# Kernel optimization log

Hardware: AMD Instinct MI355X
Metric: run time of the kernel (lower is better)

The kernel has to match this reference:

```python
import jax, jax.numpy as jnp
import numpy as np

N, E, F, D, L, G, T = 100000, 600000, 64, 128, 3, 256, 10
BN_EPS = 1e-5


def _bn(x, g, b):
    # training-mode BatchNorm1d over all rows (biased variance)
    m = x.mean(0)
    v = jnp.mean((x - m) ** 2, 0)
    return (x - m) * jax.lax.rsqrt(v + BN_EPS) * g + b


def _masked_bn(x, mask, g, b):
    # BatchNorm1d computed only over rows where mask==1 (target nodes),
    # matching torch's nn(s[target_nodes_id]) which normalizes the subset.
    cnt = jnp.maximum(mask.sum(), 1.0)
    m = (mask[:, None] * x).sum(0) / cnt
    v = (mask[:, None] * (x - m) ** 2).sum(0) / cnt
    return (x - m) * jax.lax.rsqrt(v + BN_EPS) * g + b


def setup_inputs() -> dict:
    key = jax.random.key(0)
    ks = jax.random.split(key, 32)
    inp = {}
    inp["dag_x"] = jax.random.normal(ks[0], (N, F), dtype=jnp.float32)
    inp["dag_edge_index"] = jax.random.randint(ks[1], (2, E), 0, N)
    inp["edge_multiplicities"] = jax.random.uniform(ks[2], (E,), dtype=jnp.float32)
    inp["dag_layers_mask"] = jax.random.randint(ks[3], (E,), 0, L)
    inp["batch"] = jnp.sort(jax.random.randint(ks[4], (N,), 0, G))
    inp["leaves0"] = jax.random.randint(ks[5], (50000,), 0, N)
    inp["readouts"] = jax.random.randint(ks[6], (L + 1, 20000), 0, N)
    # node_features_transformation params
    inp["W1"] = jax.random.normal(ks[7], (F, D), dtype=jnp.float32) / np.sqrt(F)
    inp["b1"] = jnp.zeros((D,), jnp.float32)
    inp["g1"] = jnp.ones((D,), jnp.float32)
    inp["be1"] = jnp.zeros((D,), jnp.float32)
    inp["W2"] = jax.random.normal(ks[8], (D, D), dtype=jnp.float32) / np.sqrt(D)
    inp["b2"] = jnp.zeros((D,), jnp.float32)
    inp["g2"] = jnp.ones((D,), jnp.float32)
    inp["be2"] = jnp.zeros((D,), jnp.float32)
    # per-DAG-layer MLP params (stacked over L layers)
    inp["dag_W1"] = jax.random.normal(ks[9], (L, D, D), dtype=jnp.float32) / np.sqrt(D)
    inp["dag_b1"] = jnp.zeros((L, D), jnp.float32)
    inp["dag_g1"] = jnp.ones((L, D), jnp.float32)
    inp["dag_be1"] = jnp.zeros((L, D), jnp.float32)
    inp["dag_W2"] = jax.random.normal(ks[10], (L, D, D), dtype=jnp.float32) / np.sqrt(D)
    inp["dag_b2"] = jnp.zeros((L, D), jnp.float32)
    inp["dag_g2"] = jnp.ones((L, D), jnp.float32)
    inp["dag_be2"] = jnp.zeros((L, D), jnp.float32)
    inp["dag_eps"] = jnp.zeros((L,), jnp.float32)
    # readout linear (last_layer)
    inp["Wl"] = jax.random.normal(ks[11], (D, T), dtype=jnp.float32) / np.sqrt(D)
    inp["bl"] = jnp.zeros((T,), jnp.float32)
    return inp


def reference(dag_x, edge_multiplicities, W1, b1, g1, be1, W2, b2, g2, be2,
              dag_W1, dag_b1, dag_g1, dag_be1, dag_W2, dag_b2, dag_g2, dag_be2,
              dag_eps, Wl, bl, dag_edge_index, dag_layers_mask, batch, leaves0,
              readouts):
    # node feature transformation: Linear-BN-ReLU x2
    feature = jax.nn.relu(_bn(dag_x @ W1 + b1, g1, be1))
    feature = jax.nn.relu(_bn(feature @ W2 + b2, g2, be2))
    # x starts as zeros except on layer-0 leaves
    x = jnp.zeros_like(feature).at[leaves0].set(feature[leaves0])
    src, dst = dag_edge_index[0], dag_edge_index[1]
    for i in range(L):
        active = (dag_layers_mask == i)
        w = jnp.where(active, edge_multiplicities, 0.0)  # [E]
        # weighted gather-scatter message passing (inactive edges contribute 0)
        E_X = jax.ops.segment_sum(x[src] * w[:, None], dst, num_segments=N)
        tcnt = jax.ops.segment_sum(active.astype(jnp.float32), dst, num_segments=N)
        is_t = (tcnt > 0).astype(x.dtype)  # [N] target-node mask
        # self-loop term (1+eps)*feature only on targets, plus aggregated messages
        s = is_t[:, None] * ((1.0 + dag_eps[i]) * feature) + E_X
        h = jax.nn.relu(_masked_bn(s @ dag_W1[i] + dag_b1[i], is_t, dag_g1[i], dag_be1[i]))
        h = jax.nn.relu(_masked_bn(h @ dag_W2[i] + dag_b2[i], is_t, dag_g2[i], dag_be2[i]))
        # MLP applied only on target nodes, then residual add of x
        x = jnp.where(is_t[:, None] > 0, h, s) + x
    # multi-height readout: sum-pool per graph at each height, then mean over heights
    pooled = []
    for i in range(L + 1):
        idx = readouts[i]
        pooled.append(jax.ops.segment_sum(x[idx], batch[idx], num_segments=G))
    out = jnp.stack(pooled, 1).mean(1) @ Wl + bl  # [G, T]
    return out
```

## Files before the change

kernel.cpp:

```cpp
#include <hip/hip_runtime.h>

constexpr int Nn = 100000;
constexpr int Ee = 600000;
constexpr int Dd = 128;
constexpr int Ll = 3;
constexpr int Gg = 256;
constexpr int Tt = 10;
constexpr float BN_EPS = 1e-5f;
constexpr int NREP = 16;
constexpr int PSL = 8;
constexpr int PR = 32;

typedef __attribute__((ext_vector_type(8))) short short8v;
typedef __attribute__((ext_vector_type(4))) float f32x4;

__device__ inline ushort bf_hi(float f) {
  unsigned u = __float_as_uint(f);
  unsigned r = (u + 0x7FFFu + ((u >> 16) & 1u)) >> 16;
  return (ushort)r;
}
__device__ inline float bf_f(ushort h) {
  return __uint_as_float(((unsigned)h) << 16);
}

__device__ inline void compute_ss_lds(const float* __restrict__ stats,
                                      const float* __restrict__ g,
                                      const float* __restrict__ be, float cnt,
                                      float* ssS) {
  const int c = threadIdx.x;
  if (c < 128) {
    float S = 0.f, Q = 0.f;
#pragma unroll
    for (int r = 0; r < NREP; ++r) {
      S += stats[r * 512 + c];
      Q += stats[r * 512 + 256 + c];
    }
    const float m = S / cnt;
    const float v = Q / cnt - m * m;
    const float sc = g[c] * rsqrtf(v + BN_EPS);
    ssS[c] = sc;
    ssS[128 + c] = be[c] - m * sc;
  }
}

template <bool NORM_A, bool MASKED>
__global__ __launch_bounds__(256, 4) void gemm_bf16(
    const ushort* __restrict__ A, const ushort* __restrict__ WTh,
    const ushort* __restrict__ WTl, const float* __restrict__ bias,
    const float* __restrict__ statsIn, const float* __restrict__ gN,
    const float* __restrict__ beN, const float* __restrict__ cntPtr,
    const int* __restrict__ tmask, ushort* __restrict__ C,
    float* __restrict__ statsOut, int nrows) {
  __shared__ ushort SB[16384];
  __shared__ float ssS[256];
  ushort* Bh = SB;
  ushort* Bl = SB + 8192;
  const int tid = threadIdx.x;
  const int w = tid >> 6, lane = tid & 63, lr = lane & 15, lg = lane >> 4;
  const int rt = blockIdx.x >> 1, ct = blockIdx.x & 1;
  const int rowBase = rt * 128, cBase = ct * 64;
  const int rep = blockIdx.x & (NREP - 1);

  {
    const int cc = tid >> 2;
    const ushort* sH = WTh + (size_t)(cBase + cc) * 128;
    const ushort* sL = WTl + (size_t)(cBase + cc) * 128;
    char* BhB = (char*)Bh;
    char* BlB = (char*)Bl;
#pragma unroll
    for (int i = 0; i < 4; ++i) {
      const int slot = (tid & 3) * 4 + i;
      const int off = (cc * 256 + slot * 16) ^ ((cc & 7) << 4);
      *(short8v*)(BhB + off) = *(const short8v*)(sH + slot * 8);
      *(short8v*)(BlB + off) = *(const short8v*)(sL + slot * 8);
    }
  }
  if (NORM_A) {
    const float cnt = cntPtr ? fmaxf(cntPtr[0], 1.f) : (float)nrows;
    compute_ss_lds(statsIn, gN, beN, cnt, ssS);
  }

  const int row0 = rowBase + w * 32 + lr;
  const int row1 = row0 + 16;
  const bool ok0 = row0 < nrows, ok1 = row1 < nrows;
  const short8v szero = {0, 0, 0, 0, 0, 0, 0, 0};
  const ushort* aP0 = A + (size_t)row0 * 128 + lg * 8;
  const ushort* aP1 = A + (size_t)row1 * 128 + lg * 8;
  short8v ar0[4], ar1[4];
#pragma unroll
  for (int c = 0; c < 4; ++c) {
    ar0[c] = ok0 ? *(const short8v*)(aP0 + c * 32) : szero;
    ar1[c] = ok1 ? *(const short8v*)(aP1 + c * 32) : szero;
  }
  __syncthreads();

  const f32x4 fzero = {0.f, 0.f, 0.f, 0.f};
  f32x4 acc[2][4];
#pragma unroll
  for (int i = 0; i < 2; ++i)
#pragma unroll
    for (int j = 0; j < 4; ++j) acc[i][j] = fzero;

  const char* BhB = (const char*)Bh;
  const char* BlB = (const char*)Bl;
  __builtin_amdgcn_s_setprio(1);
#pragma unroll
  for (int c = 0; c < 4; ++c) {
    short8v a0 = ar0[c], a1 = ar1[c];
    if (NORM_A) {
      const int kb = c * 32 + lg * 8;
      const float4 s0 = *(const float4*)&ssS[kb];
      const float4 s1 = *(const float4*)&ssS[kb + 4];
      const float4 h0 = *(const float4*)&ssS[128 + kb];
      const float4 h1 = *(const float4*)&ssS[128 + kb + 4];
      const float sv[8] = {s0.x, s0.y, s0.z, s0.w, s1.x, s1.y, s1.z, s1.w};
      const float hv[8] = {h0.x, h0.y, h0.z, h0.w, h1.x, h1.y, h1.z, h1.w};
#pragma unroll
      for (int j = 0; j < 8; ++j) {
        a0[j] = (short)bf_hi(fmaxf(fmaf(bf_f((ushort)a0[j]), sv[j], hv[j]), 0.f));
        a1[j] = (short)bf_hi(fmaxf(fmaf(bf_f((ushort)a1[j]), sv[j], hv[j]), 0.f));
      }
    }
#pragma unroll
    for (int nf = 0; nf < 4; ++nf) {
      const int brow = nf * 16 + lr;
      const int off = (brow * 256 + (c * 4 + lg) * 16) ^ ((lr & 7) << 4);
      const short8v bh = *(const short8v*)(BhB + off);
      const short8v bl = *(const short8v*)(BlB + off);
      acc[0][nf] = __builtin_amdgcn_mfma_f32_16x16x32_bf16(a0, bh, acc[0][nf], 0, 0, 0);
      acc[1][nf] = __builtin_amdgcn_mfma_f32_16x16x32_bf16(a1, bh, acc[1][nf], 0, 0, 0);
      acc[0][nf] = __builtin_amdgcn_mfma_f32_16x16x32_bf16(a0, bl, acc[0][nf], 0, 0, 0);
      acc[1][nf] = __builtin_amdgcn_mfma_f32_16x16x32_bf16(a1, bl, acc[1][nf], 0, 0, 0);
    }
  }
  __builtin_amdgcn_s_setprio(0);

  float mrow[2][4];
#pragma unroll
  for (int mf = 0; mf < 2; ++mf)
#pragma unroll
    for (int rr = 0; rr < 4; ++rr) {
      const int row = rowBase + w * 32 + mf * 16 + lg * 4 + rr;
      float m = 0.f;
      if (row < nrows) m = MASKED ? ((tmask[row] > 0) ? 1.f : 0.f) : 1.f;
      mrow[mf][rr] = m;
    }
  __syncthreads();
  ushort* Cs = SB;
  float* Sred = (float*)(SB + 9216);
  float* Sq = Sred + 256;
#pragma unroll
  for (int nf = 0; nf < 4; ++nf) {
    const int col = nf * 16 + lr;
    const float bcol = bias[cBase + col];
    float ps = 0.f, pq = 0.f;
#pragma unroll
    for (int mf = 0; mf < 2; ++mf) {
      const f32x4 vv = acc[mf][nf];
#pragma unroll
      for (int rr = 0; rr < 4; ++rr) {
        const float o = vv[rr] + bcol;
        const int rl = w * 32 + mf * 16 + lg * 4 + rr;
        Cs[rl * 72 + col] = bf_hi(o);
        const float mo = mrow[mf][rr] * o;
        ps += mo;
        pq += mo * o;
      }
    }
    ps += __shfl_xor(ps, 16);
    ps += __shfl_xor(ps, 32);
    pq += __shfl_xor(pq, 16);
    pq += __shfl_xor(pq, 32);
    if (lg == 0) {
      Sred[w * 64 + col] = ps;
      Sq[w * 64 + col] = pq;
    }
  }
  __syncthreads();
  {
    const int rl = tid >> 1, half = tid & 1;
    const int grow = rowBase + rl;
    if (grow < nrows) {
      ushort* dstp = C + (size_t)grow * 128 + cBase + half * 32;
      const ushort* srcp = Cs + rl * 72 + half * 32;
#pragma unroll
      for (int j = 0; j < 4; ++j)
        *(short8v*)(dstp + j * 8) = *(const short8v*)(srcp + j * 8);
    }
  }
  if (tid < 64) {
    float s = 0.f;
#pragma unroll
    for (int q = 0; q < 4; ++q) s += Sred[q * 64 + tid];
    atomicAdd(&statsOut[rep * 512 + cBase + tid], s);
  } else if (tid < 128) {
    float s = 0.f;
#pragma unroll
    for (int q = 0; q < 4; ++q) s += Sq[q * 64 + tid - 64];
    atomicAdd(&statsOut[rep * 512 + 256 + cBase + tid - 64], s);
  }
}

__global__ __launch_bounds__(256, 4) void gemm_f32a(
    const float* __restrict__ A, const ushort* __restrict__ WTh,
    const ushort* __restrict__ WTl, const float* __restrict__ bias,
    ushort* __restrict__ C, float* __restrict__ statsOut, int nrows) {
  __shared__ ushort SB[11264];
  ushort* Bh = SB;
  ushort* Bl = SB + 4096;
  const int tid = threadIdx.x;
  const int w = tid >> 6, lane = tid & 63, lr = lane & 15, lg = lane >> 4;
  const int rt = blockIdx.x >> 1, ct = blockIdx.x & 1;
  const int rowBase = rt * 128, cBase = ct * 64;
  const int rep = blockIdx.x & (NREP - 1);

  {
    const int cc = tid >> 2;
    const ushort* sH = WTh + (size_t)(cBase + cc) * 64;
    const ushort* sL = WTl + (size_t)(cBase + cc) * 64;
    char* BhB = (char*)Bh;
    char* BlB = (char*)Bl;
#pragma unroll
    for (int i = 0; i < 2; ++i) {
      const int slot = (tid & 3) * 2 + i;
      const int off = (cc * 128 + slot * 16) ^ ((cc & 7) << 4);
      *(short8v*)(BhB + off) = *(const short8v*)(sH + slot * 8);
      *(short8v*)(BlB + off) = *(const short8v*)(sL + slot * 8);
    }
  }

  const int row0 = rowBase + w * 32 + lr;
  const int row1 = row0 + 16;
  const bool ok0 = row0 < nrows, ok1 = row1 < nrows;
  const float4 fz4 = make_float4(0.f, 0.f, 0.f, 0.f);
  const float* aP0 = A + (size_t)row0 * 64 + lg * 8;
  const float* aP1 = A + (size_t)row1 * 64 + lg * 8;
  float4 ar0[2][2], ar1[2][2];
#pragma unroll
  for (int c = 0; c < 2; ++c) {
    ar0[c][0] = ok0 ? *(const float4*)(aP0 + c * 32) : fz4;
    ar0[c][1] = ok0 ? *(const float4*)(aP0 + c * 32 + 4) : fz4;
    ar1[c][0] = ok1 ? *(const float4*)(aP1 + c * 32) : fz4;
    ar1[c][1] = ok1 ? *(const float4*)(aP1 + c * 32 + 4) : fz4;
  }
  __syncthreads();

  const f32x4 fzero = {0.f, 0.f, 0.f, 0.f};
  f32x4 acc[2][4];
#pragma unroll
  for (int i = 0; i < 2; ++i)
#pragma unroll
    for (int j = 0; j < 4; ++j) acc[i][j] = fzero;

  const char* BhB = (const char*)Bh;
  const char* BlB = (const char*)Bl;
  __builtin_amdgcn_s_setprio(1);
#pragma unroll
  for (int c = 0; c < 2; ++c) {
    const float v0[8] = {ar0[c][0].x, ar0[c][0].y, ar0[c][0].z, ar0[c][0].w,
                         ar0[c][1].x, ar0[c][1].y, ar0[c][1].z, ar0[c][1].w};
    const float v1[8] = {ar1[c][0].x, ar1[c][0].y, ar1[c][0].z, ar1[c][0].w,
                         ar1[c][1].x, ar1[c][1].y, ar1[c][1].z, ar1[c][1].w};
    short8v a0h, a0l, a1h, a1l;
#pragma unroll
    for (int j = 0; j < 8; ++j) {
      ushort hh = bf_hi(v0[j]);
      a0h[j] = (short)hh;
      a0l[j] = (short)bf_hi(v0[j] - bf_f(hh));
      hh = bf_hi(v1[j]);
      a1h[j] = (short)hh;
      a1l[j] = (short)bf_hi(v1[j] - bf_f(hh));
    }
#pragma unroll
    for (int nf = 0; nf < 4; ++nf) {
      const int brow = nf * 16 + lr;
      const int off = (brow * 128 + (c * 4 + lg) * 16) ^ ((lr & 7) << 4);
      const short8v bh = *(const short8v*)(BhB + off);
      const short8v bl = *(const short8v*)(BlB + off);
      acc[0][nf] = __builtin_amdgcn_mfma_f32_16x16x32_bf16(a0h, bh, acc[0][nf], 0, 0, 0);
      acc[1][nf] = __builtin_amdgcn_mfma_f32_16x16x32_bf16(a1h, bh, acc[1][nf], 0, 0, 0);
      acc[0][nf] = __builtin_amdgcn_mfma_f32_16x16x32_bf16(a0l, bh, acc[0][nf], 0, 0, 0);
      acc[1][nf] = __builtin_amdgcn_mfma_f32_16x16x32_bf16(a1l, bh, acc[1][nf], 0, 0, 0);
      acc[0][nf] = __builtin_amdgcn_mfma_f32_16x16x32_bf16(a0h, bl, acc[0][nf], 0, 0, 0);
      acc[1][nf] = __builtin_amdgcn_mfma_f32_16x16x32_bf16(a1h, bl, acc[1][nf], 0, 0, 0);
    }
  }
  __builtin_amdgcn_s_setprio(0);

  __syncthreads();
  ushort* Cs = SB;
  float* Sred = (float*)(SB + 9216);
  float* Sq = Sred + 256;
#pragma unroll
  for (int nf = 0; nf < 4; ++nf) {
    const int col = nf * 16 + lr;
    const float bcol = bias[cBase + col];
    float ps = 0.f, pq = 0.f;
#pragma unroll
    for (int mf = 0; mf < 2; ++mf) {
      const f32x4 vv = acc[mf][nf];
#pragma unroll
      for (int rr = 0; rr < 4; ++rr) {
        const float o = vv[rr] + bcol;
        const int rl = w * 32 + mf * 16 + lg * 4 + rr;
        Cs[rl * 72 + col] = bf_hi(o);
        const int row = rowBase + rl;
        const float m = (row < nrows) ? 1.f : 0.f;
        const float mo = m * o;
        ps += mo;
        pq += mo * o;
      }
    }
    ps += __shfl_xor(ps, 16);
    ps += __shfl_xor(ps, 32);
    pq += __shfl_xor(pq, 16);
    pq += __shfl_xor(pq, 32);
    if (lg == 0) {
      Sred[w * 64 + col] = ps;
      Sq[w * 64 + col] = pq;
    }
  }
  __syncthreads();
  {
    const int rl = tid >> 1, half = tid & 1;
    const int grow = rowBase + rl;
    if (grow < nrows) {
      ushort* dstp = C + (size_t)grow * 128 + cBase + half * 32;
      const ushort* srcp = Cs + rl * 72 + half * 32;
#pragma unroll
      for (int j = 0; j < 4; ++j)
        *(short8v*)(dstp + j * 8) = *(const short8v*)(srcp + j * 8);
    }
  }
  if (tid < 64) {
    float s = 0.f;
#pragma unroll
    for (int q = 0; q < 4; ++q) s += Sred[q * 64 + tid];
    atomicAdd(&statsOut[rep * 512 + cBase + tid], s);
  } else if (tid < 128) {
    float s = 0.f;
#pragma unroll
    for (int q = 0; q < 4; ++q) s += Sq[q * 64 + tid - 64];
    atomicAdd(&statsOut[rep * 512 + 256 + cBase + tid - 64], s);
  }
}

__global__ __launch_bounds__(256) void wsplit_kernel(
    const float* __restrict__ W1, const float* __restrict__ W2,
    const float* __restrict__ dW1, const float* __restrict__ dW2,
    ushort* __restrict__ wsT) {
  const int t = blockIdx.x * 256 + threadIdx.x;
  const int slot = t >> 14;
  const int idx = t & 16383;
  if (slot >= 8) return;
  const int Ks = (slot == 0) ? 64 : 128;
  if (idx >= 128 * Ks) return;
  const int c = idx / Ks;
  const int k = idx - c * Ks;
  float v;
  if (slot == 0) v = W1[k * 128 + c];
  else if (slot == 1) v = W2[k * 128 + c];
  else if (slot < 5) v = dW1[(slot - 2) * 16384 + k * 128 + c];
  else v = dW2[(slot - 5) * 16384 + k * 128 + c];
  const ushort h = bf_hi(v);
  const ushort l = bf_hi(v - bf_f(h));
  wsT[slot * 32768 + c * Ks + k] = h;
  wsT[slot * 32768 + 16384 + c * Ks + k] = l;
}

__global__ __launch_bounds__(256) void normrelu_kernel(
    const ushort* __restrict__ in, const float* __restrict__ stats,
    const float* __restrict__ g, const float* __restrict__ be, float cntFixed,
    ushort* __restrict__ outp) {
  __shared__ float ssS[256];
  compute_ss_lds(stats, g, be, cntFixed, ssS);
  __syncthreads();
  const int tid = threadIdx.x;
  const int c4 = (tid & 31) * 4;
  const float4 sc = *(const float4*)&ssS[c4];
  const float4 sh = *(const float4*)&ssS[128 + c4];
  const int rowBase = blockIdx.x * 64;
#pragma unroll
  for (int it = 0; it < 8; ++it) {
    const int row = rowBase + it * 8 + (tid >> 5);
    if (row >= Nn) continue;
    const size_t idx = (size_t)row * 32 + (tid & 31);
    const ushort4 v = ((const ushort4*)in)[idx];
    ushort4 o;
    o.x = bf_hi(fmaxf(fmaf(bf_f(v.x), sc.x, sh.x), 0.f));
    o.y = bf_hi(fmaxf(fmaf(bf_f(v.y), sc.y, sh.y), 0.f));
    o.z = bf_hi(fmaxf(fmaf(bf_f(v.z), sc.z, sh.z), 0.f));
    o.w = bf_hi(fmaxf(fmaf(bf_f(v.w), sc.w, sh.w), 0.f));
    ((ushort4*)outp)[idx] = o;
  }
}

__global__ __launch_bounds__(256) void normrelu_acc_kernel(
    const ushort* __restrict__ in, const float* __restrict__ stats,
    const float* __restrict__ g, const float* __restrict__ be,
    const float* __restrict__ cntPtr, const int* __restrict__ tmask,
    ushort* __restrict__ x) {
  __shared__ float ssS[256];
  compute_ss_lds(stats, g, be, fmaxf(cntPtr[0], 1.f), ssS);
  __syncthreads();
  const int tid = threadIdx.x;
  const int c4 = (tid & 31) * 4;
  const float4 sc = *(const float4*)&ssS[c4];
  const float4 sh = *(const float4*)&ssS[128 + c4];
  const int rowBase = blockIdx.x * 64;
#pragma unroll
  for (int it = 0; it < 8; ++it) {
    const int row = rowBase + it * 8 + (tid >> 5);
    if (row >= Nn || tmask[row] <= 0) continue;
    const size_t idx = (size_t)row * 32 + (tid & 31);
    const ushort4 v = ((const ushort4*)in)[idx];
    ushort4 xo = ((const ushort4*)x)[idx];
    xo.x = bf_hi(bf_f(xo.x) + fmaxf(fmaf(bf_f(v.x), sc.x, sh.x), 0.f));
    xo.y = bf_hi(bf_f(xo.y) + fmaxf(fmaf(bf_f(v.y), sc.y, sh.y), 0.f));
    xo.z = bf_hi(bf_f(xo.z) + fmaxf(fmaf(bf_f(v.z), sc.z, sh.z), 0.f));
    xo.w = bf_hi(bf_f(xo.w) + fmaxf(fmaf(bf_f(v.w), sc.w, sh.w), 0.f));
    ((ushort4*)x)[idx] = xo;
  }
}

__global__ __launch_bounds__(256) void scatter_leaves_kernel(
    const int* __restrict__ leaves, const ushort* __restrict__ feat,
    ushort* __restrict__ x, int nl) {
  const int gid = blockIdx.x * 256 + threadIdx.x;
  const int j = gid >> 5;
  if (j >= nl) return;
  const int node = leaves[j];
  const int c4 = (gid & 31) * 4;
  *(ushort4*)&x[(size_t)node * 128 + c4] =
      *(const ushort4*)&feat[(size_t)node * 128 + c4];
}

__global__ __launch_bounds__(256) void deg_count_kernel(
    const int* __restrict__ dst, const int* __restrict__ lmask,
    int* __restrict__ cnts) {
  const int e = blockIdx.x * 256 + threadIdx.x;
  if (e >= Ee) return;
  atomicAdd(&cnts[lmask[e] * Nn + dst[e]], 1);
}

__global__ __launch_bounds__(256) void scan1_kernel(const int* __restrict__ in,
                                                    int* __restrict__ out,
                                                    int* __restrict__ bsum,
                                                    float* __restrict__ tcountf,
                                                    int n) {
  __shared__ int lds[256];
  __shared__ float tcS[3];
  const int tid = threadIdx.x;
  const int base = blockIdx.x * 2048 + tid * 8;
  int vals[8];
  int tsum = 0;
  float t0 = 0.f, t1 = 0.f, t2 = 0.f;
#pragma unroll
  for (int j = 0; j < 8; ++j) {
    const int i = base + j;
    const int v = (i < n) ? in[i] : 0;
    if (v > 0) {
      if (i < Nn) t0 += 1.f;
      else if (i < 2 * Nn) t1 += 1.f;
      else t2 += 1.f;
    }
    vals[j] = tsum;
    tsum += v;
  }
  lds[tid] = tsum;
  if (tid < 3) tcS[tid] = 0.f;
  __syncthreads();
  if (t0 != 0.f) atomicAdd(&tcS[0], t0);
  if (t1 != 0.f) atomicAdd(&tcS[1], t1);
  if (t2 != 0.f) atomicAdd(&tcS[2], t2);
  for (int off = 1; off < 256; off <<= 1) {
    const int y = (tid >= off) ? lds[tid - off] : 0;
    __syncthreads();
    lds[tid] += y;
    __syncthreads();
  }
  const int texcl = (tid > 0) ? lds[tid - 1] : 0;
#pragma unroll
  for (int j = 0; j < 8; ++j)
    if (base + j < n) out[base + j] = texcl + vals[j];
  if (tid == 255) bsum[blockIdx.x] = lds[255];
  __syncthreads();
  if (tid < 3 && tcS[tid] != 0.f) atomicAdd(&tcountf[tid], tcS[tid]);
}

__global__ void scan2_kernel(int* __restrict__ bsum, int nb) {
  __shared__ int lds[256];
  const int tid = threadIdx.x;
  const int v = (tid < nb) ? bsum[tid] : 0;
  lds[tid] = v;
  __syncthreads();
  for (int off = 1; off < 256; off <<= 1) {
    const int y = (tid >= off) ? lds[tid - off] : 0;
    __syncthreads();
    lds[tid] += y;
    __syncthreads();
  }
  if (tid < nb) bsum[tid] = lds[tid] - v;
}

__global__ __launch_bounds__(256) void scan3_kernel(int* __restrict__ out,
                                                    int* __restrict__ cursor,
                                                    const int* __restrict__ bsum,
                                                    int n, int etot) {
  const int i = blockIdx.x * 256 + threadIdx.x;
  if (i >= n) return;
  const int v = out[i] + bsum[i >> 11];
  out[i] = v;
  cursor[i] = v;
  if (i == n - 1) out[n] = etot;
}

__global__ __launch_bounds__(256) void csr_fill_kernel(
    const int* __restrict__ src, const int* __restrict__ dst,
    const float* __restrict__ mult, const int* __restrict__ lmask,
    int* __restrict__ cursor, int2* __restrict__ pairs) {
  const int e = blockIdx.x * 256 + threadIdx.x;
  if (e >= Ee) return;
  const int slot = atomicAdd(&cursor[lmask[e] * Nn + dst[e]], 1);
  pairs[slot] = make_int2(src[e], __float_as_int(mult[e]));
}

__global__ __launch_bounds__(256) void agg_kernel(
    const int* __restrict__ offs, const int2* __restrict__ pairs,
    const ushort* __restrict__ x, const ushort* __restrict__ feat,
    const float* __restrict__ deps, int layer, ushort* __restrict__ sbuf,
    int* __restrict__ tmask) {
  const int node = blockIdx.x * 4 + (threadIdx.x >> 6);
  const int lane = threadIdx.x & 63;
  const int gi = layer * Nn + node;
  const int o0 = offs[gi];
  const int o1 = offs[gi + 1];
  ushort2 fv = make_ushort2(0, 0);
  if (o1 > o0) fv = *(const ushort2*)&feat[(size_t)node * 128 + lane * 2];
  float ax = 0.f, ay = 0.f;
  for (int p = o0; p < o1; p += 2) {
    const int2 pr0 = pairs[p];
    const int2 pr1 = (p + 1 < o1) ? pairs[p + 1] : make_int2(0, 0);
    const ushort2 x0 = *(const ushort2*)&x[(size_t)pr0.x * 128 + lane * 2];
    const ushort2 x1 = *(const ushort2*)&x[(size_t)pr1.x * 128 + lane * 2];
    const float w0 = __int_as_float(pr0.y);
    const float w1 = __int_as_float(pr1.y);
    ax = fmaf(w0, bf_f(x0.x), ax);
    ay = fmaf(w0, bf_f(x0.y), ay);
    ax = fmaf(w1, bf_f(x1.x), ax);
    ay = fmaf(w1, bf_f(x1.y), ay);
  }
  if (o1 > o0) {
    const float c = 1.f + deps[layer];
    ax = fmaf(c, bf_f(fv.x), ax);
    ay = fmaf(c, bf_f(fv.y), ay);
  }
  ushort2 o;
  o.x = bf_hi(ax);
  o.y = bf_hi(ay);
  *(ushort2*)&sbuf[(size_t)node * 128 + lane * 2] = o;
  if (lane == 0) tmask[node] = (o1 > o0) ? 1 : 0;
}

__global__ __launch_bounds__(256) void phist_kernel(const int* __restrict__ ridx,
                                                    const int* __restrict__ batch,
                                                    int* __restrict__ cnt, int n) {
  const int i = blockIdx.x * 256 + threadIdx.x;
  if (i >= n) return;
  atomicAdd(&cnt[batch[ridx[i]] * PR + (i & (PR - 1))], 1);
}

__global__ void pscan_kernel(int* __restrict__ cnt, int* __restrict__ cur) {
  __shared__ int l[256];
  const int t = threadIdx.x;
  const int base = t * 32;
  int vals[32];
  int tsum = 0;
#pragma unroll
  for (int j = 0; j < 32; ++j) {
    const int v = cnt[base + j];
    vals[j] = tsum;
    tsum += v;
  }
  l[t] = tsum;
  __syncthreads();
  for (int off = 1; off < 256; off <<= 1) {
    const int y = (t >= off) ? l[t - off] : 0;
    __syncthreads();
    l[t] += y;
    __syncthreads();
  }
  const int excl = (t > 0) ? l[t - 1] : 0;
#pragma unroll
  for (int j = 0; j < 32; ++j) {
    const int v = excl + vals[j];
    cnt[base + j] = v;
    cur[base + j] = v;
  }
}

__global__ __launch_bounds__(256) void pfill_kernel(const int* __restrict__ ridx,
                                                    const int* __restrict__ batch,
                                                    int* __restrict__ cur,
                                                    int* __restrict__ sorted,
                                                    int n) {
  const int i = blockIdx.x * 256 + threadIdx.x;
  if (i >= n) return;
  const int node = ridx[i];
  const int slot = atomicAdd(&cur[batch[node] * PR + (i & (PR - 1))], 1);
  sorted[slot] = node;
}

__global__ __launch_bounds__(256) void ppool_kernel(const int* __restrict__ sorted,
                                                    const int* __restrict__ offs,
                                                    const ushort* __restrict__ x,
                                                    float* __restrict__ Ppart,
                                                    int n) {
  __shared__ float part[4][256];
  const int bid = blockIdx.x;
  const int g = bid >> 3, slice = bid & (PSL - 1);
  const int w = threadIdx.x >> 6;
  const int lane = threadIdx.x & 63;
  const int o0 = offs[g * PR];
  const int o1 = (g < Gg - 1) ? offs[(g + 1) * PR] : n;
  float ax = 0.f, ay = 0.f;
  for (int p = o0 + slice * 4 + w; p < o1; p += 32) {
    const int node = sorted[p];
    const ushort2 xv = *(const ushort2*)&x[(size_t)node * 128 + lane * 2];
    ax += bf_f(xv.x);
    ay += bf_f(xv.y);
  }
  part[w][lane * 2] = ax;
  part[w][lane * 2 + 1] = ay;
  __syncthreads();
  if (threadIdx.x < 128) {
    const int c = threadIdx.x;
    Ppart[(size_t)bid * 128 + c] =
        part[0][c] + part[1][c] + part[2][c] + part[3][c];
  }
}

__global__ __launch_bounds__(256) void preduce_kernel(
    const float* __restrict__ Ppart, float* __restrict__ P) {
  const int gid = blockIdx.x * 256 + threadIdx.x;
  const int g = gid >> 7, c = gid & 127;
  float s = 0.f;
#pragma unroll
  for (int t = 0; t < PSL; ++t) s += Ppart[(size_t)(g * PSL + t) * 128 + c];
  P[gid] = s;
}

__global__ void out_kernel(const float* __restrict__ P,
                           const float* __restrict__ Wl,
                           const float* __restrict__ bl,
                           float* __restrict__ out) {
  const int gid = blockIdx.x * blockDim.x + threadIdx.x;
  if (gid >= Gg * Tt) return;
  const int g = gid / Tt;
  const int t = gid - g * Tt;
  float acc = 0.f;
  for (int c = 0; c < 128; ++c) acc += P[g * 128 + c] * Wl[c * Tt + t];
  out[gid] = acc * 0.25f + bl[t];
}

extern "C" void kernel_launch(void* const* d_in, const int* in_sizes, int n_in,
                              void* d_out, int out_size, void* d_ws,
                              size_t ws_size, hipStream_t stream) {
  const float* dag_x = (const float*)d_in[0];
  const int* eidx = (const int*)d_in[1];
  const int* src = eidx;
  const int* dst = eidx + Ee;
  const float* mult = (const float*)d_in[2];
  const int* lmask = (const int*)d_in[3];
  const int* batch = (const int*)d_in[4];
  const int* leaves = (const int*)d_in[5];
  const int* readouts = (const int*)d_in[6];
  const float* W1 = (const float*)d_in[7];
  const float* b1 = (const float*)d_in[8];
  const float* g1 = (const float*)d_in[9];
  const float* be1 = (const float*)d_in[10];
  const float* W2 = (const float*)d_in[11];
  const float* b2 = (const float*)d_in[12];
  const float* g2 = (const float*)d_in[13];
  const float* be2 = (const float*)d_in[14];
  const float* dW1 = (const float*)d_in[15];
  const float* db1 = (const float*)d_in[16];
  const float* dg1 = (const float*)d_in[17];
  const float* dbe1 = (const float*)d_in[18];
  const float* dW2 = (const float*)d_in[19];
  const float* db2 = (const float*)d_in[20];
  const float* dg2 = (const float*)d_in[21];
  const float* dbe2 = (const float*)d_in[22];
  const float* deps = (const float*)d_in[23];
  const float* Wl = (const float*)d_in[24];
  const float* bl = (const float*)d_in[25];
  float* out = (float*)d_out;

  const size_t ND = (size_t)Nn * Dd;
  ushort* feat = (ushort*)d_ws;
  ushort* xbuf = feat + ND;
  ushort* Abuf = xbuf + ND;
  ushort* Bbuf = Abuf + ND;
  float* statsAll = (float*)(Bbuf + ND);
  float* tcountf = statsAll + 8 * 8192;
  int* tmask = (int*)(tcountf + 8);
  ushort* wsT = (ushort*)(tmask + Nn);
  int* offs = (int*)(wsT + 262144);
  int2* pairs = (int2*)(offs + 3 * Nn + 4);

  int* cnts = (int*)xbuf;
  int* cursor = cnts + 3 * Nn;
  int* bsum = cursor + 3 * Nn;
  const int nridx = in_sizes[6];
  const int nleaves = in_sizes[5];
  int* pcnt = (int*)Abuf;
  int* pcur = pcnt + Gg * PR;
  int* sorted = pcur + Gg * PR;
  float* Ppart = (float*)(sorted + nridx);
  float* P = Ppart + Gg * PSL * 128;

  dim3 blk(256);
  hipMemsetAsync(statsAll, 0, (8 * 8192 + 8) * sizeof(float), stream);
  wsplit_kernel<<<512, blk, 0, stream>>>(W1, W2, dW1, dW2, wsT);

  hipMemsetAsync(cnts, 0, 3 * Nn * sizeof(int), stream);
  deg_count_kernel<<<2344, blk, 0, stream>>>(dst, lmask, cnts);
  scan1_kernel<<<147, blk, 0, stream>>>(cnts, offs, bsum, tcountf, 3 * Nn);
  scan2_kernel<<<1, blk, 0, stream>>>(bsum, 147);
  scan3_kernel<<<1172, blk, 0, stream>>>(offs, cursor, bsum, 3 * Nn, Ee);
  csr_fill_kernel<<<2344, blk, 0, stream>>>(src, dst, mult, lmask, cursor, pairs);

  const int gGemm = 782 * 2;
  gemm_f32a<<<gGemm, blk, 0, stream>>>(dag_x, wsT, wsT + 16384, b1, Abuf,
                                       statsAll + 0 * 8192, Nn);
  gemm_bf16<true, false><<<gGemm, blk, 0, stream>>>(
      Abuf, wsT + 32768, wsT + 32768 + 16384, b2, statsAll + 0 * 8192, g1, be1,
      nullptr, nullptr, Bbuf, statsAll + 1 * 8192, Nn);
  normrelu_kernel<<<1563, blk, 0, stream>>>(Bbuf, statsAll + 1 * 8192, g2, be2,
                                            (float)Nn, feat);

  hipMemsetAsync(xbuf, 0, ND * sizeof(ushort), stream);
  scatter_leaves_kernel<<<6250, blk, 0, stream>>>(leaves, feat, xbuf, nleaves);

  for (int layer = 0; layer < Ll; ++layer) {
    agg_kernel<<<25000, blk, 0, stream>>>(offs, pairs, xbuf, feat, deps, layer,
                                          Abuf, tmask);
    const int so1 = (2 + layer) * 32768;
    const int so2 = (5 + layer) * 32768;
    const int po = layer * Dd;
    float* st1 = statsAll + (size_t)(2 + 2 * layer) * 8192;
    float* st2 = statsAll + (size_t)(3 + 2 * layer) * 8192;
    gemm_bf16<false, true><<<gGemm, blk, 0, stream>>>(
        Abuf, wsT + so1, wsT + so1 + 16384, db1 + po, nullptr, nullptr,
        nullptr, nullptr, tmask, Bbuf, st1, Nn);
    gemm_bf16<true, true><<<gGemm, blk, 0, stream>>>(
        Bbuf, wsT + so2, wsT + so2 + 16384, db2 + po, st1, dg1 + po, dbe1 + po,
        tcountf + layer, tmask, Abuf, st2, Nn);
    normrelu_acc_kernel<<<1563, blk, 0, stream>>>(
        Abuf, st2, dg2 + po, dbe2 + po, tcountf + layer, tmask, xbuf);
  }

  hipMemsetAsync(pcnt, 0, Gg * PR * sizeof(int), stream);
  const int gIdx = (nridx + 255) / 256;
  phist_kernel<<<gIdx, blk, 0, stream>>>(readouts, batch, pcnt, nridx);
  pscan_kernel<<<1, blk, 0, stream>>>(pcnt, pcur);
  pfill_kernel<<<gIdx, blk, 0, stream>>>(readouts, batch, pcur, sorted, nridx);
  ppool_kernel<<<Gg * PSL, blk, 0, stream>>>(sorted, pcnt, xbuf, Ppart, nridx);
  preduce_kernel<<<Gg * 128 / 256, blk, 0, stream>>>(Ppart, P);
  out_kernel<<<10, blk, 0, stream>>>(P, Wl, bl, out);
}
```

Measured before the change: 498.2 us.

## Fuse neighbor aggregation into first DAG GEMM and merge small scan/output kernels

Adds a gemm_agg kernel that gathers weighted neighbor rows and the self-loop term directly into MFMA A-fragments in registers, replacing the separate agg_kernel and its write and re-read of the aggregated buffer. It also folds the xbuf zeroing into normrelu_kernel, merges scan2 into scan3 (each block redoes the small block-sum scan), and fuses preduce and out_kernel into one pout_kernel. These changes remove intermediate global traffic and several launches. In exchange, each GEMM block does irregular gathers with one lane-group per row, which may load-imbalance and stall the MFMA pipeline on high-degree nodes.

```diff
diff --git a/kernel.cpp b/kernel.cpp
--- a/kernel.cpp
+++ b/kernel.cpp
@@ -144,6 +144,222 @@
       float m = 0.f;
       if (row < nrows) m = MASKED ? ((tmask[row] > 0) ? 1.f : 0.f) : 1.f;
       mrow[mf][rr] = m;
+    }
+  __syncthreads();
+  ushort* Cs = SB;
+  float* Sred = (float*)(SB + 9216);
+  float* Sq = Sred + 256;
+#pragma unroll
+  for (int nf = 0; nf < 4; ++nf) {
+    const int col = nf * 16 + lr;
+    const float bcol = bias[cBase + col];
+    float ps = 0.f, pq = 0.f;
+#pragma unroll
+    for (int mf = 0; mf < 2; ++mf) {
+      const f32x4 vv = acc[mf][nf];
+#pragma unroll
+      for (int rr = 0; rr < 4; ++rr) {
+        const float o = vv[rr] + bcol;
+        const int rl = w * 32 + mf * 16 + lg * 4 + rr;
+        Cs[rl * 72 + col] = bf_hi(o);
+        const float mo = mrow[mf][rr] * o;
+        ps += mo;
+        pq += mo * o;
+      }
+    }
+    ps += __shfl_xor(ps, 16);
+    ps += __shfl_xor(ps, 32);
+    pq += __shfl_xor(pq, 16);
+    pq += __shfl_xor(pq, 32);
+    if (lg == 0) {
+      Sred[w * 64 + col] = ps;
+      Sq[w * 64 + col] = pq;
+    }
+  }
+  __syncthreads();
+  {
+    const int rl = tid >> 1, half = tid & 1;
+    const int grow = rowBase + rl;
+    if (grow < nrows) {
+      ushort* dstp = C + (size_t)grow * 128 + cBase + half * 32;
+      const ushort* srcp = Cs + rl * 72 + half * 32;
+#pragma unroll
+      for (int j = 0; j < 4; ++j)
+        *(short8v*)(dstp + j * 8) = *(const short8v*)(srcp + j * 8);
+    }
+  }
+  if (tid < 64) {
+    float s = 0.f;
+#pragma unroll
+    for (int q = 0; q < 4; ++q) s += Sred[q * 64 + tid];
+    atomicAdd(&statsOut[rep * 512 + cBase + tid], s);
+  } else if (tid < 128) {
+    float s = 0.f;
+#pragma unroll
+    for (int q = 0; q < 4; ++q) s += Sq[q * 64 + tid - 64];
+    atomicAdd(&statsOut[rep * 512 + 256 + cBase + tid - 64], s);
+  }
+}
+
+__global__ __launch_bounds__(256, 4) void gemm_agg(
+    const ushort* __restrict__ x, const ushort* __restrict__ feat,
+    const int* __restrict__ offs, const int2* __restrict__ pairs,
+    const float* __restrict__ deps, int layer, const ushort* __restrict__ WTh,
+    const ushort* __restrict__ WTl, const float* __restrict__ bias,
+    ushort* __restrict__ C, float* __restrict__ statsOut,
+    int* __restrict__ tmask, int nrows) {
+  __shared__ ushort SB[16384];
+  ushort* Bh = SB;
+  ushort* Bl = SB + 8192;
+  const int tid = threadIdx.x;
+  const int w = tid >> 6, lane = tid & 63, lr = lane & 15, lg = lane >> 4;
+  const int rt = blockIdx.x >> 1, ct = blockIdx.x & 1;
+  const int rowBase = rt * 128, cBase = ct * 64;
+  const int rep = blockIdx.x & (NREP - 1);
+
+  {
+    const int cc = tid >> 2;
+    const ushort* sH = WTh + (size_t)(cBase + cc) * 128;
+    const ushort* sL = WTl + (size_t)(cBase + cc) * 128;
+    char* BhB = (char*)Bh;
+    char* BlB = (char*)Bl;
+#pragma unroll
+    for (int i = 0; i < 4; ++i) {
+      const int slot = (tid & 3) * 4 + i;
+      const int off = (cc * 256 + slot * 16) ^ ((cc & 7) << 4);
+      *(short8v*)(BhB + off) = *(const short8v*)(sH + slot * 8);
+      *(short8v*)(BlB + off) = *(const short8v*)(sL + slot * 8);
+    }
+  }
+
+  const float ce = 1.f + deps[layer];
+  const int row0 = rowBase + w * 32 + lr;
+  const int row1 = row0 + 16;
+  int o0a = 0, o1a = 0, o0b = 0, o1b = 0;
+  if (row0 < nrows) {
+    o0a = offs[layer * Nn + row0];
+    o1a = offs[layer * Nn + row0 + 1];
+  }
+  if (row1 < nrows) {
+    o0b = offs[layer * Nn + row1];
+    o1b = offs[layer * Nn + row1 + 1];
+  }
+  if (lg == 0) {
+    if (row0 < nrows) tmask[row0] = (o1a > o0a) ? 1 : 0;
+    if (row1 < nrows) tmask[row1] = (o1b > o0b) ? 1 : 0;
+  }
+
+  short8v ar0[4], ar1[4];
+  {
+    float a[4][8];
+#pragma unroll
+    for (int c = 0; c < 4; ++c)
+#pragma unroll
+      for (int j = 0; j < 8; ++j) a[c][j] = 0.f;
+    for (int p = o0a; p < o1a; ++p) {
+      const int2 pr = pairs[p];
+      const float wgt = __int_as_float(pr.y);
+      const ushort* xr = x + (size_t)pr.x * 128 + lg * 8;
+#pragma unroll
+      for (int c = 0; c < 4; ++c) {
+        const short8v xv = *(const short8v*)(xr + c * 32);
+#pragma unroll
+        for (int j = 0; j < 8; ++j)
+          a[c][j] = fmaf(wgt, bf_f((ushort)xv[j]), a[c][j]);
+      }
+    }
+    if (o1a > o0a) {
+      const ushort* fr = feat + (size_t)row0 * 128 + lg * 8;
+#pragma unroll
+      for (int c = 0; c < 4; ++c) {
+        const short8v fv = *(const short8v*)(fr + c * 32);
+#pragma unroll
+        for (int j = 0; j < 8; ++j)
+          a[c][j] = fmaf(ce, bf_f((ushort)fv[j]), a[c][j]);
+      }
+    }
+#pragma unroll
+    for (int c = 0; c < 4; ++c)
+#pragma unroll
+      for (int j = 0; j < 8; ++j) ar0[c][j] = (short)bf_hi(a[c][j]);
+  }
+  {
+    float a[4][8];
+#pragma unroll
+    for (int c = 0; c < 4; ++c)
+#pragma unroll
+      for (int j = 0; j < 8; ++j) a[c][j] = 0.f;
+    for (int p = o0b; p < o1b; ++p) {
+      const int2 pr = pairs[p];
+      const float wgt = __int_as_float(pr.y);
+      const ushort* xr = x + (size_t)pr.x * 128 + lg * 8;
+#pragma unroll
+      for (int c = 0; c < 4; ++c) {
+        const short8v xv = *(const short8v*)(xr + c * 32);
+#pragma unroll
+        for (int j = 0; j < 8; ++j)
+          a[c][j] = fmaf(wgt, bf_f((ushort)xv[j]), a[c][j]);
+      }
+    }
+    if (o1b > o0b) {
+      const ushort* fr = feat + (size_t)row1 * 128 + lg * 8;
+#pragma unroll
+      for (int c = 0; c < 4; ++c) {
+        const short8v fv = *(const short8v*)(fr + c * 32);
+#pragma unroll
+        for (int j = 0; j < 8; ++j)
+          a[c][j] = fmaf(ce, bf_f((ushort)fv[j]), a[c][j]);
+      }
+    }
+#pragma unroll
+    for (int c = 0; c < 4; ++c)
+#pragma unroll
+      for (int j = 0; j < 8; ++j) ar1[c][j] = (short)bf_hi(a[c][j]);
+  }
+  __syncthreads();
+
+  const f32x4 fzero = {0.f, 0.f, 0.f, 0.f};
+  f32x4 acc[2][4];
+#pragma unroll
+  for (int i = 0; i < 2; ++i)
+#pragma unroll
+    for (int j = 0; j < 4; ++j) acc[i][j] = fzero;
+
+  const char* BhB = (const char*)Bh;
+  const char* BlB = (const char*)Bl;
+  __builtin_amdgcn_s_setprio(1);
+#pragma unroll
+  for (int c = 0; c < 4; ++c) {
+    const short8v a0 = ar0[c], a1 = ar1[c];
+#pragma unroll
+    for (int nf = 0; nf < 4; ++nf) {
+      const int brow = nf * 16 + lr;
+      const int off = (brow * 256 + (c * 4 + lg) * 16) ^ ((lr & 7) << 4);
+      const short8v bh = *(const short8v*)(BhB + off);
+      const short8v bl = *(const short8v*)(BlB + off);
+      acc[0][nf] = __builtin_amdgcn_mfma_f32_16x16x32_bf16(a0, bh, acc[0][nf], 0, 0, 0);
+      acc[1][nf] = __builtin_amdgcn_mfma_f32_16x16x32_bf16(a1, bh, acc[1][nf], 0, 0, 0);
+      acc[0][nf] = __builtin_amdgcn_mfma_f32_16x16x32_bf16(a0, bl, acc[0][nf], 0, 0, 0);
+      acc[1][nf] = __builtin_amdgcn_mfma_f32_16x16x32_bf16(a1, bl, acc[1][nf], 0, 0, 0);
+    }
+  }
+  __builtin_amdgcn_s_setprio(0);
+
+  const float dga = (o1a > o0a) ? 1.f : 0.f;
+  const float dgb = (o1b > o0b) ? 1.f : 0.f;
+  float mrow[2][4];
+#pragma unroll
+  for (int rr = 0; rr < 4; ++rr) {
+    const int srcl = lg * 4 + rr;
+    mrow[0][rr] = __shfl(dga, (w << 6 & 0) + srcl, 64);
+    mrow[1][rr] = __shfl(dgb, srcl, 64);
+  }
+#pragma unroll
+  for (int mf = 0; mf < 2; ++mf)
+#pragma unroll
+    for (int rr = 0; rr < 4; ++rr) {
+      const int row = rowBase + w * 32 + mf * 16 + lg * 4 + rr;
+      if (row >= nrows) mrow[mf][rr] = 0.f;
     }
   __syncthreads();
   ushort* Cs = SB;
@@ -371,7 +587,7 @@
 __global__ __launch_bounds__(256) void normrelu_kernel(
     const ushort* __restrict__ in, const float* __restrict__ stats,
     const float* __restrict__ g, const float* __restrict__ be, float cntFixed,
-    ushort* __restrict__ outp) {
+    ushort* __restrict__ outp, ushort* __restrict__ xz) {
   __shared__ float ssS[256];
   compute_ss_lds(stats, g, be, cntFixed, ssS);
   __syncthreads();
@@ -380,6 +596,7 @@
   const float4 sc = *(const float4*)&ssS[c4];
   const float4 sh = *(const float4*)&ssS[128 + c4];
   const int rowBase = blockIdx.x * 64;
+  const ushort4 z4 = make_ushort4(0, 0, 0, 0);
 #pragma unroll
   for (int it = 0; it < 8; ++it) {
     const int row = rowBase + it * 8 + (tid >> 5);
@@ -392,6 +609,7 @@
     o.z = bf_hi(fmaxf(fmaf(bf_f(v.z), sc.z, sh.z), 0.f));
     o.w = bf_hi(fmaxf(fmaf(bf_f(v.w), sc.w, sh.w), 0.f));
     ((ushort4*)outp)[idx] = o;
+    ((ushort4*)xz)[idx] = z4;
   }
 }
 
@@ -488,30 +706,28 @@
   if (tid < 3 && tcS[tid] != 0.f) atomicAdd(&tcountf[tid], tcS[tid]);
 }
 
-__global__ void scan2_kernel(int* __restrict__ bsum, int nb) {
-  __shared__ int lds[256];
-  const int tid = threadIdx.x;
-  const int v = (tid < nb) ? bsum[tid] : 0;
-  lds[tid] = v;
-  __syncthreads();
-  for (int off = 1; off < 256; off <<= 1) {
-    const int y = (tid >= off) ? lds[tid - off] : 0;
-    __syncthreads();
-    lds[tid] += y;
-    __syncthreads();
-  }
-  if (tid < nb) bsum[tid] = lds[tid] - v;
-}
-
 __global__ __launch_bounds__(256) void scan3_kernel(int* __restrict__ out,
                                                     int* __restrict__ cursor,
                                                     const int* __restrict__ bsum,
-                                                    int n, int etot) {
-  const int i = blockIdx.x * 256 + threadIdx.x;
+                                                    int nb, int n, int etot) {
+  __shared__ int bs[256];
+  const int tid = threadIdx.x;
+  const int v = (tid < nb) ? bsum[tid] : 0;
+  bs[tid] = v;
+  __syncthreads();
+  for (int off = 1; off < 256; off <<= 1) {
+    const int y = (tid >= off) ? bs[tid - off] : 0;
+    __syncthreads();
+    bs[tid] += y;
+    __syncthreads();
+  }
+  const int i = blockIdx.x * 256 + tid;
   if (i >= n) return;
-  const int v = out[i] + bsum[i >> 11];
-  out[i] = v;
-  cursor[i] = v;
+  const int b = i >> 11;
+  const int excl = (b > 0) ? bs[b - 1] : 0;
+  const int val = out[i] + excl;
+  out[i] = val;
+  cursor[i] = val;
   if (i == n - 1) out[n] = etot;
 }
 
@@ -523,43 +739,6 @@
   if (e >= Ee) return;
   const int slot = atomicAdd(&cursor[lmask[e] * Nn + dst[e]], 1);
   pairs[slot] = make_int2(src[e], __float_as_int(mult[e]));
-}
-
-__global__ __launch_bounds__(256) void agg_kernel(
-    const int* __restrict__ offs, const int2* __restrict__ pairs,
-    const ushort* __restrict__ x, const ushort* __restrict__ feat,
-    const float* __restrict__ deps, int layer, ushort* __restrict__ sbuf,
-    int* __restrict__ tmask) {
-  const int node = blockIdx.x * 4 + (threadIdx.x >> 6);
-  const int lane = threadIdx.x & 63;
-  const int gi = layer * Nn + node;
-  const int o0 = offs[gi];
-  const int o1 = offs[gi + 1];
-  ushort2 fv = make_ushort2(0, 0);
-  if (o1 > o0) fv = *(const ushort2*)&feat[(size_t)node * 128 + lane * 2];
-  float ax = 0.f, ay = 0.f;
-  for (int p = o0; p < o1; p += 2) {
-    const int2 pr0 = pairs[p];
-    const int2 pr1 = (p + 1 < o1) ? pairs[p + 1] : make_int2(0, 0);
-    const ushort2 x0 = *(const ushort2*)&x[(size_t)pr0.x * 128 + lane * 2];
-    const ushort2 x1 = *(const ushort2*)&x[(size_t)pr1.x * 128 + lane * 2];
-    const float w0 = __int_as_float(pr0.y);
-    const float w1 = __int_as_float(pr1.y);
-    ax = fmaf(w0, bf_f(x0.x), ax);
-    ay = fmaf(w0, bf_f(x0.y), ay);
-    ax = fmaf(w1, bf_f(x1.x), ax);
-    ay = fmaf(w1, bf_f(x1.y), ay);
-  }
-  if (o1 > o0) {
-    const float c = 1.f + deps[layer];
-    ax = fmaf(c, bf_f(fv.x), ax);
-    ay = fmaf(c, bf_f(fv.y), ay);
-  }
-  ushort2 o;
-  o.x = bf_hi(ax);
-  o.y = bf_hi(ay);
-  *(ushort2*)&sbuf[(size_t)node * 128 + lane * 2] = o;
-  if (lane == 0) tmask[node] = (o1 > o0) ? 1 : 0;
 }
 
 __global__ __launch_bounds__(256) void phist_kernel(const int* __restrict__ ridx,
@@ -640,27 +819,22 @@
   }
 }
 
-__global__ __launch_bounds__(256) void preduce_kernel(
-    const float* __restrict__ Ppart, float* __restrict__ P) {
-  const int gid = blockIdx.x * 256 + threadIdx.x;
-  const int g = gid >> 7, c = gid & 127;
+__global__ __launch_bounds__(128) void pout_kernel(
+    const float* __restrict__ Ppart, const float* __restrict__ Wl,
+    const float* __restrict__ bl, float* __restrict__ out) {
+  __shared__ float Pl[128];
+  const int g = blockIdx.x;
+  const int t = threadIdx.x;
   float s = 0.f;
 #pragma unroll
-  for (int t = 0; t < PSL; ++t) s += Ppart[(size_t)(g * PSL + t) * 128 + c];
-  P[gid] = s;
-}
-
-__global__ void out_kernel(const float* __restrict__ P,
-                           const float* __restrict__ Wl,
-                           const float* __restrict__ bl,
-                           float* __restrict__ out) {
-  const int gid = blockIdx.x * blockDim.x + threadIdx.x;
-  if (gid >= Gg * Tt) return;
-  const int g = gid / Tt;
-  const int t = gid - g * Tt;
-  float acc = 0.f;
-  for (int c = 0; c < 128; ++c) acc += P[g * 128 + c] * Wl[c * Tt + t];
-  out[gid] = acc * 0.25f + bl[t];
+  for (int r = 0; r < PSL; ++r) s += Ppart[(size_t)(g * PSL + r) * 128 + t];
+  Pl[t] = s * 0.25f;
+  __syncthreads();
+  if (t < Tt) {
+    float acc = 0.f;
+    for (int c = 0; c < 128; ++c) acc += Pl[c] * Wl[c * Tt + t];
+    out[g * Tt + t] = acc + bl[t];
+  }
 }
 
 extern "C" void kernel_launch(void* const* d_in, const int* in_sizes, int n_in,
@@ -717,7 +891,6 @@
   int* pcur = pcnt + Gg * PR;
   int* sorted = pcur + Gg * PR;
   float* Ppart = (float*)(sorted + nridx);
-  float* P = Ppart + Gg * PSL * 128;
 
   dim3 blk(256);
   hipMemsetAsync(statsAll, 0, (8 * 8192 + 8) * sizeof(float), stream);
@@ -726,8 +899,7 @@
   hipMemsetAsync(cnts, 0, 3 * Nn * sizeof(int), stream);
   deg_count_kernel<<<2344, blk, 0, stream>>>(dst, lmask, cnts);
   scan1_kernel<<<147, blk, 0, stream>>>(cnts, offs, bsum, tcountf, 3 * Nn);
-  scan2_kernel<<<1, blk, 0, stream>>>(bsum, 147);
-  scan3_kernel<<<1172, blk, 0, stream>>>(offs, cursor, bsum, 3 * Nn, Ee);
+  scan3_kernel<<<1172, blk, 0, stream>>>(offs, cursor, bsum, 147, 3 * Nn, Ee);
   csr_fill_kernel<<<2344, blk, 0, stream>>>(src, dst, mult, lmask, cursor, pairs);
 
   const int gGemm = 782 * 2;
@@ -737,22 +909,18 @@
       Abuf, wsT + 32768, wsT + 32768 + 16384, b2, statsAll + 0 * 8192, g1, be1,
       nullptr, nullptr, Bbuf, statsAll + 1 * 8192, Nn);
   normrelu_kernel<<<1563, blk, 0, stream>>>(Bbuf, statsAll + 1 * 8192, g2, be2,
-                                            (float)Nn, feat);
-
-  hipMemsetAsync(xbuf, 0, ND * sizeof(ushort), stream);
+                                            (float)Nn, feat, xbuf);
   scatter_leaves_kernel<<<6250, blk, 0, stream>>>(leaves, feat, xbuf, nleaves);
 
   for (int layer = 0; layer < Ll; ++layer) {
-    agg_kernel<<<25000, blk, 0, stream>>>(offs, pairs, xbuf, feat, deps, layer,
-                                          Abuf, tmask);
     const int so1 = (2 + layer) * 32768;
     const int so2 = (5 + layer) * 32768;
     const int po = layer * Dd;
     float* st1 = statsAll + (size_t)(2 + 2 * layer) * 8192;
     float* st2 = statsAll + (size_t)(3 + 2 * layer) * 8192;
-    gemm_bf16<false, true><<<gGemm, blk, 0, stream>>>(
-        Abuf, wsT + so1, wsT + so1 + 16384, db1 + po, nullptr, nullptr,
-        nullptr, nullptr, tmask, Bbuf, st1, Nn);
+    gemm_agg<<<gGemm, blk, 0, stream>>>(xbuf, feat, offs, pairs, deps, layer,
+                                        wsT + so1, wsT + so1 + 16384, db1 + po,
+                                        Bbuf, st1, tmask, Nn);
     gemm_bf16<true, true><<<gGemm, blk, 0, stream>>>(
         Bbuf, wsT + so2, wsT + so2 + 16384, db2 + po, st1, dg1 + po, dbe1 + po,
         tcountf + layer, tmask, Abuf, st2, Nn);
@@ -766,6 +934,5 @@
   pscan_kernel<<<1, blk, 0, stream>>>(pcnt, pcur);
   pfill_kernel<<<gIdx, blk, 0, stream>>>(readouts, batch, pcur, sorted, nridx);
   ppool_kernel<<<Gg * PSL, blk, 0, stream>>>(sorted, pcnt, xbuf, Ppart, nridx);
-  preduce_kernel<<<Gg * 128 / 256, blk, 0, stream>>>(Ppart, P);
-  out_kernel<<<10, blk, 0, stream>>>(P, Wl, bl, out);
-}
+  pout_kernel<<<Gg, dim3(128), 0, stream>>>(Ppart, Wl, bl, out);
+}
```

New measurement: 460.7 us. 1.08x faster.
